# Kernel optimization log

Hardware: AMD Instinct MI355X
Metric: run time of the kernel (lower is better)

The kernel has to match this reference:

```python
import jax, jax.numpy as jnp
import numpy as np

N_NODES = 100000
N_EDGES = 1200000
NFEAT = 64
NHID = 64
NCLASS = 16
BN_EPS = 1e-5
L2_EPS = 1e-12


def setup_inputs() -> dict:
    key = jax.random.key(0)
    ks = jax.random.split(key, 8)
    edge_index = jax.random.randint(ks[0], (2, N_EDGES), 0, N_NODES, dtype=jnp.int64)
    x = jax.random.normal(ks[1], (N_NODES, NFEAT), dtype=jnp.float32)
    # SAGEConv params: lin_l (neighbor path, has bias), lin_r (root path, no bias)
    W_l = jax.random.normal(ks[2], (NHID, NFEAT), dtype=jnp.float32) * (1.0 / np.sqrt(NFEAT))
    b_l = jnp.zeros((NHID,), dtype=jnp.float32)
    W_r = jax.random.normal(ks[3], (NHID, NFEAT), dtype=jnp.float32) * (1.0 / np.sqrt(NFEAT))
    # BatchNorm1d affine params
    gamma = jnp.ones((NHID,), dtype=jnp.float32)
    beta = jnp.zeros((NHID,), dtype=jnp.float32)
    # final fc (xavier-ish scale, zero bias per weights_init)
    W_fc = jax.random.normal(ks[4], (NCLASS, NHID), dtype=jnp.float32) * (1.0 / np.sqrt(NHID))
    b_fc = jnp.zeros((NCLASS,), dtype=jnp.float32)
    return {"edge_index": edge_index, "x": x, "W_l": W_l, "b_l": b_l,
            "W_r": W_r, "gamma": gamma, "beta": beta, "W_fc": W_fc, "b_fc": b_fc}


def reference(edge_index, x, W_l, b_l, W_r, gamma, beta, W_fc, b_fc):
    N = x.shape[0]
    src, dst = edge_index[0], edge_index[1]
    # SAGEConv mean aggregation: gather x at source nodes, scatter-mean to dst
    msgs = x[src]                                                  # [E, F]
    sums = jax.ops.segment_sum(msgs, dst, num_segments=N)         # [N, F]
    cnt = jax.ops.segment_sum(jnp.ones((src.shape[0], 1), x.dtype), dst, num_segments=N)
    mean = sums / jnp.maximum(cnt, 1.0)
    # out = lin_l(mean_neighbors) + lin_r(x_root)
    h = mean @ W_l.T + b_l + x @ W_r.T                              # [N, H]
    # normalize=True -> L2 normalize rows (F.normalize semantics)
    h = h / jnp.maximum(jnp.linalg.norm(h, axis=-1, keepdims=True), L2_EPS)
    # transition: ReLU -> BatchNorm1d (training stats) -> Dropout (identity in eval)
    h = jax.nn.relu(h)
    mu = jnp.mean(h, axis=0)
    var = jnp.var(h, axis=0)
    h = (h - mu) / jnp.sqrt(var + BN_EPS) * gamma + beta
    return h @ W_fc.T + b_fc                                        # [N, C]
```

## Files before the change

### kernel.cpp

```cpp
#include <hip/hip_runtime.h>
#include <hip/hip_bf16.h>


typedef __attribute__((ext_vector_type(8))) short short8;
typedef __attribute__((ext_vector_type(4))) float f32x4;

__device__ __forceinline__ unsigned short f2bf(float f) {
    unsigned int u = __builtin_bit_cast(unsigned int, f);
    u += 0x7FFFu + ((u >> 16) & 1u);
    return (unsigned short)(u >> 16);
}
__device__ __forceinline__ float bf2f(unsigned short s) {
    return __builtin_bit_cast(float, ((unsigned int)s) << 16);
}

#define CHUNK 8192

__global__ __launch_bounds__(256) void k_bhist(const int* __restrict__ eidx,
                                               int* __restrict__ cnt,
                                               int E, int NB) {
    __shared__ int lh[256];
    const int tid = threadIdx.x;
    lh[tid] = 0;
    __syncthreads();
    const int base = blockIdx.x * CHUNK;
    for (int i = tid; i < CHUNK; i += 256) {
        int e = base + i;
        if (e < E) atomicAdd(&lh[eidx[E + e] >> 9], 1);
    }
    __syncthreads();
    if (tid < NB) cnt[(size_t)blockIdx.x * NB + tid] = lh[tid];
}

__global__ __launch_bounds__(256) void k_bscanA(int* __restrict__ cnt,
                                                int* __restrict__ btot,
                                                int NBLK, int NB) {
    __shared__ int swv[4];
    const int b = blockIdx.x;
    const int t = threadIdx.x;
    int v = (t < NBLK) ? cnt[(size_t)t * NB + b] : 0;
    const int lane = t & 63, wid = t >> 6;
    int s = v;
#pragma unroll
    for (int off = 1; off < 64; off <<= 1) {
        int tt = __shfl_up(s, off);
        if (lane >= off) s += tt;
    }
    if (lane == 63) swv[wid] = s;
    __syncthreads();
    if (t == 0) {
        int a = 0;
#pragma unroll
        for (int w = 0; w < 4; ++w) { int tt = swv[w]; swv[w] = a; a += tt; }
    }
    __syncthreads();
    int excl = s - v + swv[wid];
    if (t < NBLK) cnt[(size_t)t * NB + b] = excl;
    if (t == NBLK - 1) btot[b] = excl + v;
}

__global__ __launch_bounds__(256) void k_bscanB(const int* __restrict__ btot,
                                                int* __restrict__ bbase,
                                                int* __restrict__ rowptr,
                                                int NB, int N, int E) {
    __shared__ int swv[4];
    const int t = threadIdx.x;
    int v = (t < NB) ? btot[t] : 0;
    const int lane = t & 63, wid = t >> 6;
    int s = v;
#pragma unroll
    for (int off = 1; off < 64; off <<= 1) {
        int tt = __shfl_up(s, off);
        if (lane >= off) s += tt;
    }
    if (lane == 63) swv[wid] = s;
    __syncthreads();
    if (t == 0) {
        int a = 0;
#pragma unroll
        for (int w = 0; w < 4; ++w) { int tt = swv[w]; swv[w] = a; a += tt; }
    }
    __syncthreads();
    if (t < NB) bbase[t] = s - v + swv[wid];
    if (t == 0) { bbase[NB] = E; rowptr[N] = E; }
}

__global__ __launch_bounds__(256) void k_bscatter(const int* __restrict__ eidx,
                                                  const int* __restrict__ cnt,
                                                  const int* __restrict__ bbase,
                                                  unsigned int* __restrict__ ebuf,
                                                  int E, int NB) {
    __shared__ int cur[256];
    const int tid = threadIdx.x;
    if (tid < NB) cur[tid] = bbase[tid] + cnt[(size_t)blockIdx.x * NB + tid];
    __syncthreads();
    const int base = blockIdx.x * CHUNK;
    for (int i = tid; i < CHUNK; i += 256) {
        int e = base + i;
        if (e < E) {
            int d = eidx[E + e];
            int s = eidx[e];
            int p = atomicAdd(&cur[d >> 9], 1);
            ebuf[p] = (unsigned int)s | ((unsigned int)(d & 511) << 17);
        }
    }
}

__global__ __launch_bounds__(256) void k_bfinal(const unsigned int* __restrict__ ebuf,
                                                const int* __restrict__ bbase,
                                                int* __restrict__ rowptr,
                                                int* __restrict__ colv, int N) {
    __shared__ int h[512];
    __shared__ int swv[4];
    const int b = blockIdx.x;
    const int tid = threadIdx.x;
    h[2 * tid] = 0;
    h[2 * tid + 1] = 0;
    __syncthreads();
    const int segb = bbase[b], sege = bbase[b + 1];
    for (int i = segb + tid; i < sege; i += 256)
        atomicAdd(&h[ebuf[i] >> 17], 1);
    __syncthreads();
    int a0 = h[2 * tid], a1 = h[2 * tid + 1];
    int ts = a0 + a1;
    const int lane = tid & 63, wid = tid >> 6;
    int s = ts;
#pragma unroll
    for (int off = 1; off < 64; off <<= 1) {
        int tt = __shfl_up(s, off);
        if (lane >= off) s += tt;
    }
    if (lane == 63) swv[wid] = s;
    __syncthreads();
    if (tid == 0) {
        int a = 0;
#pragma unroll
        for (int w = 0; w < 4; ++w) { int tt = swv[w]; swv[w] = a; a += tt; }
    }
    __syncthreads();
    int excl = s - ts + swv[wid];
    h[2 * tid] = excl;
    h[2 * tid + 1] = excl + a0;
    int node = b * 512 + 2 * tid;
    if (node < N) rowptr[node] = segb + excl;
    if (node + 1 < N) rowptr[node + 1] = segb + excl + a0;
    __syncthreads();
    for (int i = segb + tid; i < sege; i += 256) {
        unsigned int u = ebuf[i];
        int p = atomicAdd(&h[u >> 17], 1);
        colv[segb + p] = (int)(u & 0x1FFFFu);
    }
}

__global__ __launch_bounds__(256) void k_xcast(const float4* __restrict__ x4,
                                               ushort4* __restrict__ xbf, int n4) {
    int t = blockIdx.x * 256 + threadIdx.x;
    if (t < n4) {
        float4 v = x4[t];
        xbf[t] = make_ushort4(f2bf(v.x), f2bf(v.y), f2bf(v.z), f2bf(v.w));
    }
}

__global__ __launch_bounds__(256) void k_gather_bf(
        const uint4* __restrict__ xbf8, const int* __restrict__ rowptr,
        const int* __restrict__ colv, uint4* __restrict__ mh8, int N) {
    int t = blockIdx.x * 256 + threadIdx.x;
    int n = t >> 3;
    int l = t & 7;
    if (n >= N) return;
    int b = rowptr[n], e = rowptr[n + 1];
    float a[8] = {0.f, 0.f, 0.f, 0.f, 0.f, 0.f, 0.f, 0.f};
    int p = b;
    for (; p + 4 <= e; p += 4) {
        int s0 = colv[p], s1 = colv[p + 1], s2 = colv[p + 2], s3 = colv[p + 3];
        uint4 v0 = xbf8[(size_t)s0 * 8 + l];
        uint4 v1 = xbf8[(size_t)s1 * 8 + l];
        uint4 v2 = xbf8[(size_t)s2 * 8 + l];
        uint4 v3 = xbf8[(size_t)s3 * 8 + l];
        unsigned int w0[4] = {v0.x, v0.y, v0.z, v0.w};
        unsigned int w1[4] = {v1.x, v1.y, v1.z, v1.w};
        unsigned int w2[4] = {v2.x, v2.y, v2.z, v2.w};
        unsigned int w3[4] = {v3.x, v3.y, v3.z, v3.w};
#pragma unroll
        for (int q = 0; q < 4; ++q) {
            a[2 * q] += bf2f((unsigned short)(w0[q] & 0xFFFF)) +
                        bf2f((unsigned short)(w1[q] & 0xFFFF)) +
                        bf2f((unsigned short)(w2[q] & 0xFFFF)) +
                        bf2f((unsigned short)(w3[q] & 0xFFFF));
            a[2 * q + 1] += bf2f((unsigned short)(w0[q] >> 16)) +
                            bf2f((unsigned short)(w1[q] >> 16)) +
                            bf2f((unsigned short)(w2[q] >> 16)) +
                            bf2f((unsigned short)(w3[q] >> 16));
        }
    }
    for (; p < e; ++p) {
        int s0 = colv[p];
        uint4 v0 = xbf8[(size_t)s0 * 8 + l];
        unsigned int w0[4] = {v0.x, v0.y, v0.z, v0.w};
#pragma unroll
        for (int q = 0; q < 4; ++q) {
            a[2 * q] += bf2f((unsigned short)(w0[q] & 0xFFFF));
            a[2 * q + 1] += bf2f((unsigned short)(w0[q] >> 16));
        }
    }
    float inv = 1.0f / fmaxf((float)(e - b), 1.0f);
    uint4 o;
    unsigned int* op = &o.x;
#pragma unroll
    for (int q = 0; q < 4; ++q) {
        unsigned int lo = f2bf(a[2 * q] * inv);
        unsigned int hi = f2bf(a[2 * q + 1] * inv);
        op[q] = lo | (hi << 16);
    }
    mh8[(size_t)n * 8 + l] = o;
}

__global__ __launch_bounds__(256) void k_gather_f32(
        const float4* __restrict__ x4, const int* __restrict__ rowptr,
        const int* __restrict__ colv, ushort4* __restrict__ mh, int N) {
    int t = blockIdx.x * 256 + threadIdx.x;
    int n = t >> 4;
    int l = t & 15;
    if (n >= N) return;
    int b = rowptr[n], e = rowptr[n + 1];
    float ax = 0.f, ay = 0.f, az = 0.f, aw = 0.f;
    int p = b;
    for (; p + 4 <= e; p += 4) {
        int s0 = colv[p], s1 = colv[p + 1], s2 = colv[p + 2], s3 = colv[p + 3];
        float4 v0 = x4[(size_t)s0 * 16 + l];
        float4 v1 = x4[(size_t)s1 * 16 + l];
        float4 v2 = x4[(size_t)s2 * 16 + l];
        float4 v3 = x4[(size_t)s3 * 16 + l];
        ax += (v0.x + v1.x) + (v2.x + v3.x);
        ay += (v0.y + v1.y) + (v2.y + v3.y);
        az += (v0.z + v1.z) + (v2.z + v3.z);
        aw += (v0.w + v1.w) + (v2.w + v3.w);
    }
    for (; p < e; ++p) {
        int s0 = colv[p];
        float4 v0 = x4[(size_t)s0 * 16 + l];
        ax += v0.x; ay += v0.y; az += v0.z; aw += v0.w;
    }
    float inv = 1.0f / fmaxf((float)(e - b), 1.0f);
    mh[(size_t)n * 16 + l] = make_ushort4(f2bf(ax * inv), f2bf(ay * inv),
                                          f2bf(az * inv), f2bf(aw * inv));
}

__global__ __launch_bounds__(256) void k_fused(
        const float* __restrict__ x,
        const float* __restrict__ Wl, const float* __restrict__ bl,
        const float* __restrict__ Wr,
        unsigned short* __restrict__ mh,
        float* __restrict__ pstats, int N) {
    __shared__ float sRed[4][128];

    const int tid = threadIdx.x;
    const int wid = tid >> 6;
    const int lane = tid & 63;
    const int l15 = lane & 15;
    const int quad = lane >> 4;
    const int tbase = blockIdx.x * 64 + wid * 16;

    short8 bfrag[4][4];
#pragma unroll
    for (int c = 0; c < 4; ++c) {
#pragma unroll
        for (int f = 0; f < 4; ++f) {
            const int n = f * 16 + l15;
            const float* wsrc = (c < 2)
                ? (Wl + (size_t)n * 64 + c * 32 + quad * 8)
                : (Wr + (size_t)n * 64 + (c - 2) * 32 + quad * 8);
            float4 w0 = *(const float4*)wsrc;
            float4 w1 = *(const float4*)(wsrc + 4);
            union { short8 v; unsigned short u[8]; } pk;
            pk.u[0] = f2bf(w0.x); pk.u[1] = f2bf(w0.y);
            pk.u[2] = f2bf(w0.z); pk.u[3] = f2bf(w0.w);
            pk.u[4] = f2bf(w1.x); pk.u[5] = f2bf(w1.y);
            pk.u[6] = f2bf(w1.z); pk.u[7] = f2bf(w1.w);
            bfrag[c][f] = pk.v;
        }
    }

    const int mrow = tbase + l15;
    const int mld = (mrow < N) ? mrow : (N - 1);
    f32x4 acc[4] = {{0.f, 0.f, 0.f, 0.f}, {0.f, 0.f, 0.f, 0.f},
                    {0.f, 0.f, 0.f, 0.f}, {0.f, 0.f, 0.f, 0.f}};
#pragma unroll
    for (int c = 0; c < 2; ++c) {
        short8 a = *(const short8*)(mh + (size_t)mld * 64 + c * 32 + quad * 8);
#pragma unroll
        for (int f = 0; f < 4; ++f)
            acc[f] = __builtin_amdgcn_mfma_f32_16x16x32_bf16(a, bfrag[c][f], acc[f], 0, 0, 0);
    }
#pragma unroll
    for (int c = 2; c < 4; ++c) {
        const float* xp = x + (size_t)mld * 64 + (c - 2) * 32 + quad * 8;
        float4 a0 = *(const float4*)xp;
        float4 a1 = *(const float4*)(xp + 4);
        union { short8 v; unsigned short u[8]; } pk;
        pk.u[0] = f2bf(a0.x); pk.u[1] = f2bf(a0.y);
        pk.u[2] = f2bf(a0.z); pk.u[3] = f2bf(a0.w);
        pk.u[4] = f2bf(a1.x); pk.u[5] = f2bf(a1.y);
        pk.u[6] = f2bf(a1.z); pk.u[7] = f2bf(a1.w);
#pragma unroll
        for (int f = 0; f < 4; ++f)
            acc[f] = __builtin_amdgcn_mfma_f32_16x16x32_bf16(pk.v, bfrag[c][f], acc[f], 0, 0, 0);
    }

    float blv[4];
#pragma unroll
    for (int f = 0; f < 4; ++f) blv[f] = bl[f * 16 + l15];

    float psum[4] = {0.f, 0.f, 0.f, 0.f};
    float psq[4] = {0.f, 0.f, 0.f, 0.f};
#pragma unroll
    for (int reg = 0; reg < 4; ++reg) {
        const int node = tbase + quad * 4 + reg;
        float hv[4];
        float ss = 0.f;
#pragma unroll
        for (int f = 0; f < 4; ++f) {
            hv[f] = acc[f][reg] + blv[f];
            ss += hv[f] * hv[f];
        }
        ss += __shfl_xor(ss, 1);
        ss += __shfl_xor(ss, 2);
        ss += __shfl_xor(ss, 4);
        ss += __shfl_xor(ss, 8);
        float sc = 1.0f / fmaxf(sqrtf(ss), 1e-12f);
        if (node < N) {
#pragma unroll
            for (int f = 0; f < 4; ++f) {
                float r = fmaxf(hv[f] * sc, 0.f);
                unsigned short rb = f2bf(r);
                float e = bf2f(rb);
                mh[(size_t)node * 64 + f * 16 + l15] = rb;
                psum[f] += e;
                psq[f] += e * e;
            }
        }
    }

#pragma unroll
    for (int f = 0; f < 4; ++f) {
        psum[f] += __shfl_xor(psum[f], 16);
        psum[f] += __shfl_xor(psum[f], 32);
        psq[f] += __shfl_xor(psq[f], 16);
        psq[f] += __shfl_xor(psq[f], 32);
    }
    if (lane < 16) {
#pragma unroll
        for (int f = 0; f < 4; ++f) {
            sRed[wid][f * 16 + l15] = psum[f];
            sRed[wid][64 + f * 16 + l15] = psq[f];
        }
    }
    __syncthreads();
    if (tid < 128) {
        float v = sRed[0][tid] + sRed[1][tid] + sRed[2][tid] + sRed[3][tid];
        pstats[(size_t)blockIdx.x * 128 + tid] = v;
    }
}

__global__ __launch_bounds__(64) void k_stats(const float* __restrict__ pstats,
                                              float* __restrict__ stats, int nblk) {
    int col = blockIdx.x;
    int l = threadIdx.x;
    float s = 0.f;
    for (int r = l; r < nblk; r += 64) s += pstats[(size_t)r * 128 + col];
    s += __shfl_xor(s, 1);
    s += __shfl_xor(s, 2);
    s += __shfl_xor(s, 4);
    s += __shfl_xor(s, 8);
    s += __shfl_xor(s, 16);
    s += __shfl_xor(s, 32);
    if (l == 0) stats[col] = s;
}

__global__ __launch_bounds__(256) void k_out(
        const unsigned short* __restrict__ h, const float* __restrict__ stats,
        const float* __restrict__ gamma, const float* __restrict__ beta,
        const float* __restrict__ Wfc, const float* __restrict__ bfc,
        float* __restrict__ out, int N) {
    __shared__ float sWm[64 * 16];
    __shared__ float sShift[64];
    __shared__ float sBase[16];
    const int tid = threadIdx.x;
    const float invN = 1.0f / (float)N;
    if (tid < 64) {
        float mu = stats[tid] * invN;
        float var = stats[64 + tid] * invN - mu * mu;
        float sc = gamma[tid] / sqrtf(var + 1e-5f);
        sShift[tid] = beta[tid] - mu * sc;
#pragma unroll
        for (int c = 0; c < 16; ++c) sWm[tid * 16 + c] = Wfc[c * 64 + tid] * sc;
    }
    __syncthreads();
    if (tid < 16) {
        float b = bfc[tid];
#pragma unroll
        for (int j = 0; j < 64; ++j) b += sShift[j] * Wfc[tid * 64 + j];
        sBase[tid] = b;
    }
    __syncthreads();
    int g = blockIdx.x * 256 + tid;
    int n = g >> 4;
    int c = g & 15;
    if (n >= N) return;
    const ushort4* h4 = (const ushort4*)(h + (size_t)n * 64);
    float acc = sBase[c];
#pragma unroll
    for (int jq = 0; jq < 16; ++jq) {
        ushort4 v = h4[jq];
        acc += bf2f(v.x) * sWm[(jq * 4 + 0) * 16 + c];
        acc += bf2f(v.y) * sWm[(jq * 4 + 1) * 16 + c];
        acc += bf2f(v.z) * sWm[(jq * 4 + 2) * 16 + c];
        acc += bf2f(v.w) * sWm[(jq * 4 + 3) * 16 + c];
    }
    out[(size_t)n * 16 + c] = acc;
}

extern "C" void kernel_launch(void* const* d_in, const int* in_sizes, int n_in,
                              void* d_out, int out_size, void* d_ws, size_t ws_size,
                              hipStream_t stream) {
    const int* eidx = (const int*)d_in[0];
    const float* x = (const float*)d_in[1];
    const float* Wl = (const float*)d_in[2];
    const float* bl = (const float*)d_in[3];
    const float* Wr = (const float*)d_in[4];
    const float* gamma = (const float*)d_in[5];
    const float* beta = (const float*)d_in[6];
    const float* Wfc = (const float*)d_in[7];
    const float* bfc = (const float*)d_in[8];
    float* out = (float*)d_out;

    const int E = in_sizes[0] / 2;
    const int N = in_sizes[1] / 64;
    const int fblocks = (N + 63) / 64;
    const int NB = (N + 511) >> 9;
    const int NBLK = (E + CHUNK - 1) / CHUNK;

    int* colv = (int*)d_ws;
    int* rowptr = colv + E;
    int* cnt = rowptr + (N + 1);
    int* btot = cnt + (size_t)NBLK * NB;
    int* bbase = btot + 256;
    float* pstats = (float*)(bbase + 257);
    float* stats = pstats + (size_t)fblocks * 128;
    unsigned short* mh = (unsigned short*)(stats + 128);
    unsigned int* tail = (unsigned int*)(mh + (size_t)N * 64);

    size_t fixed_words = (size_t)(tail - (unsigned int*)d_ws);
    const bool xbf_on = (ws_size >= (fixed_words + (size_t)N * 32) * 4);
    unsigned short* xbf = (unsigned short*)tail;
    unsigned int* ebuf = tail;

    int eblocks = (E + 255) / 256;
    k_bhist<<<NBLK, 256, 0, stream>>>(eidx, cnt, E, NB);
    k_bscanA<<<NB, 256, 0, stream>>>(cnt, btot, NBLK, NB);
    k_bscanB<<<1, 256, 0, stream>>>(btot, bbase, rowptr, NB, N, E);
    k_bscatter<<<NBLK, 256, 0, stream>>>(eidx, cnt, bbase, ebuf, E, NB);
    k_bfinal<<<NB, 256, 0, stream>>>(ebuf, bbase, rowptr, colv, N);

    if (xbf_on) {
        int cblocks = (int)(((size_t)N * 16 + 255) / 256);
        k_xcast<<<cblocks, 256, 0, stream>>>((const float4*)x, (ushort4*)xbf, N * 16);
        int gblocks = (int)(((size_t)N * 8 + 255) / 256);
        k_gather_bf<<<gblocks, 256, 0, stream>>>((const uint4*)xbf, rowptr, colv,
                                                 (uint4*)mh, N);
    } else {
        int gblocks = (int)(((size_t)N * 16 + 255) / 256);
        k_gather_f32<<<gblocks, 256, 0, stream>>>((const float4*)x, rowptr, colv,
                                                  (ushort4*)mh, N);
    }

    k_fused<<<fblocks, 256, 0, stream>>>(x, Wl, bl, Wr, mh, pstats, N);

    k_stats<<<128, 64, 0, stream>>>(pstats, stats, fblocks);

    int oblocks = (int)(((size_t)N * 16 + 255) / 256);
    k_out<<<oblocks, 256, 0, stream>>>(mh, stats, gamma, beta, Wfc, bfc, out, N);
}
```

Baseline: 236.0 us.

## Fuse CSR finalize with neighbor gather in shared memory and merge prep kernels

```diff
diff --git a/kernel.cpp b/kernel.cpp
--- a/kernel.cpp
+++ b/kernel.cpp
@@ -13,34 +13,53 @@
 __device__ __forceinline__ float bf2f(unsigned short s) {
     return __builtin_bit_cast(float, ((unsigned int)s) << 16);
 }
+__device__ __forceinline__ float bflo(unsigned int w) {
+    return __builtin_bit_cast(float, w << 16);
+}
+__device__ __forceinline__ float bfhi(unsigned int w) {
+    return __builtin_bit_cast(float, w & 0xFFFF0000u);
+}
 
 #define CHUNK 8192
-
-__global__ __launch_bounds__(256) void k_bhist(const int* __restrict__ eidx,
-                                               int* __restrict__ cnt,
-                                               int E, int NB) {
+#define MAXSEG 8192
+
+__global__ __launch_bounds__(256) void k_prep(const int* __restrict__ eidx,
+                                              int* __restrict__ cnt,
+                                              const float4* __restrict__ x4,
+                                              ushort4* __restrict__ xbf,
+                                              int E, int NB, int NBLK,
+                                              int n4, int do_x) {
     __shared__ int lh[256];
     const int tid = threadIdx.x;
-    lh[tid] = 0;
-    __syncthreads();
-    const int base = blockIdx.x * CHUNK;
-    for (int i = tid; i < CHUNK; i += 256) {
-        int e = base + i;
-        if (e < E) atomicAdd(&lh[eidx[E + e] >> 9], 1);
-    }
-    __syncthreads();
-    if (tid < NB) cnt[(size_t)blockIdx.x * NB + tid] = lh[tid];
-}
-
-__global__ __launch_bounds__(256) void k_bscanA(int* __restrict__ cnt,
-                                                int* __restrict__ btot,
-                                                int NBLK, int NB) {
+    if ((int)blockIdx.x < NBLK) {
+        lh[tid] = 0;
+        __syncthreads();
+        const int base = blockIdx.x * CHUNK;
+        for (int i = tid; i < CHUNK; i += 256) {
+            int e = base + i;
+            if (e < E) atomicAdd(&lh[eidx[E + e] >> 9], 1);
+        }
+        __syncthreads();
+        if (tid < NB) cnt[(size_t)blockIdx.x * NB + tid] = lh[tid];
+    } else if (do_x) {
+        int t = ((int)blockIdx.x - NBLK) * 256 + tid;
+        if (t < n4) {
+            float4 v = x4[t];
+            xbf[t] = make_ushort4(f2bf(v.x), f2bf(v.y), f2bf(v.z), f2bf(v.w));
+        }
+    }
+}
+
+__global__ __launch_bounds__(256) void k_bscan(int* __restrict__ cnt,
+                                               int* __restrict__ bbase,
+                                               int NBLK, int NB, int E) {
     __shared__ int swv[4];
-    const int b = blockIdx.x;
     const int t = threadIdx.x;
-    int v = (t < NBLK) ? cnt[(size_t)t * NB + b] : 0;
+    int tot = 0;
+    if (t < NB)
+        for (int c = 0; c < NBLK; ++c) tot += cnt[(size_t)c * NB + t];
     const int lane = t & 63, wid = t >> 6;
-    int s = v;
+    int s = tot;
 #pragma unroll
     for (int off = 1; off < 64; off <<= 1) {
         int tt = __shfl_up(s, off);
@@ -54,45 +73,26 @@
         for (int w = 0; w < 4; ++w) { int tt = swv[w]; swv[w] = a; a += tt; }
     }
     __syncthreads();
-    int excl = s - v + swv[wid];
-    if (t < NBLK) cnt[(size_t)t * NB + b] = excl;
-    if (t == NBLK - 1) btot[b] = excl + v;
-}
-
-__global__ __launch_bounds__(256) void k_bscanB(const int* __restrict__ btot,
-                                                int* __restrict__ bbase,
-                                                int* __restrict__ rowptr,
-                                                int NB, int N, int E) {
-    __shared__ int swv[4];
-    const int t = threadIdx.x;
-    int v = (t < NB) ? btot[t] : 0;
-    const int lane = t & 63, wid = t >> 6;
-    int s = v;
-#pragma unroll
-    for (int off = 1; off < 64; off <<= 1) {
-        int tt = __shfl_up(s, off);
-        if (lane >= off) s += tt;
-    }
-    if (lane == 63) swv[wid] = s;
-    __syncthreads();
-    if (t == 0) {
-        int a = 0;
-#pragma unroll
-        for (int w = 0; w < 4; ++w) { int tt = swv[w]; swv[w] = a; a += tt; }
-    }
-    __syncthreads();
-    if (t < NB) bbase[t] = s - v + swv[wid];
-    if (t == 0) { bbase[NB] = E; rowptr[N] = E; }
+    int base = s - tot + swv[wid];
+    if (t < NB) {
+        bbase[t] = base;
+        int run = base;
+        for (int c = 0; c < NBLK; ++c) {
+            int v = cnt[(size_t)c * NB + t];
+            cnt[(size_t)c * NB + t] = run;
+            run += v;
+        }
+    }
+    if (t == 0) bbase[NB] = E;
 }
 
 __global__ __launch_bounds__(256) void k_bscatter(const int* __restrict__ eidx,
                                                   const int* __restrict__ cnt,
-                                                  const int* __restrict__ bbase,
                                                   unsigned int* __restrict__ ebuf,
                                                   int E, int NB) {
     __shared__ int cur[256];
     const int tid = threadIdx.x;
-    if (tid < NB) cur[tid] = bbase[tid] + cnt[(size_t)blockIdx.x * NB + tid];
+    if (tid < NB) cur[tid] = cnt[(size_t)blockIdx.x * NB + tid];
     __syncthreads();
     const int base = blockIdx.x * CHUNK;
     for (int i = tid; i < CHUNK; i += 256) {
@@ -106,148 +106,125 @@
     }
 }
 
-__global__ __launch_bounds__(256) void k_bfinal(const unsigned int* __restrict__ ebuf,
+__global__ __launch_bounds__(256) void k_bucket(const unsigned int* __restrict__ ebuf,
                                                 const int* __restrict__ bbase,
-                                                int* __restrict__ rowptr,
-                                                int* __restrict__ colv, int N) {
-    __shared__ int h[512];
+                                                const uint2* __restrict__ xbf2,
+                                                const float4* __restrict__ x4,
+                                                uint2* __restrict__ mh2,
+                                                int N, int use_bf) {
+    __shared__ int lh[512];
+    __shared__ int lcur[512];
+    __shared__ int srcl[MAXSEG];
     __shared__ int swv[4];
     const int b = blockIdx.x;
     const int tid = threadIdx.x;
-    h[2 * tid] = 0;
-    h[2 * tid + 1] = 0;
-    __syncthreads();
     const int segb = bbase[b], sege = bbase[b + 1];
+    const int seg = sege - segb;
+    lh[2 * tid] = 0;
+    lh[2 * tid + 1] = 0;
+    __syncthreads();
     for (int i = segb + tid; i < sege; i += 256)
-        atomicAdd(&h[ebuf[i] >> 17], 1);
-    __syncthreads();
-    int a0 = h[2 * tid], a1 = h[2 * tid + 1];
-    int ts = a0 + a1;
-    const int lane = tid & 63, wid = tid >> 6;
-    int s = ts;
-#pragma unroll
-    for (int off = 1; off < 64; off <<= 1) {
-        int tt = __shfl_up(s, off);
-        if (lane >= off) s += tt;
-    }
-    if (lane == 63) swv[wid] = s;
-    __syncthreads();
-    if (tid == 0) {
-        int a = 0;
-#pragma unroll
-        for (int w = 0; w < 4; ++w) { int tt = swv[w]; swv[w] = a; a += tt; }
-    }
-    __syncthreads();
-    int excl = s - ts + swv[wid];
-    h[2 * tid] = excl;
-    h[2 * tid + 1] = excl + a0;
-    int node = b * 512 + 2 * tid;
-    if (node < N) rowptr[node] = segb + excl;
-    if (node + 1 < N) rowptr[node + 1] = segb + excl + a0;
-    __syncthreads();
-    for (int i = segb + tid; i < sege; i += 256) {
-        unsigned int u = ebuf[i];
-        int p = atomicAdd(&h[u >> 17], 1);
-        colv[segb + p] = (int)(u & 0x1FFFFu);
-    }
-}
-
-__global__ __launch_bounds__(256) void k_xcast(const float4* __restrict__ x4,
-                                               ushort4* __restrict__ xbf, int n4) {
-    int t = blockIdx.x * 256 + threadIdx.x;
-    if (t < n4) {
-        float4 v = x4[t];
-        xbf[t] = make_ushort4(f2bf(v.x), f2bf(v.y), f2bf(v.z), f2bf(v.w));
-    }
-}
-
-__global__ __launch_bounds__(256) void k_gather_bf(
-        const uint4* __restrict__ xbf8, const int* __restrict__ rowptr,
-        const int* __restrict__ colv, uint4* __restrict__ mh8, int N) {
-    int t = blockIdx.x * 256 + threadIdx.x;
-    int n = t >> 3;
-    int l = t & 7;
-    if (n >= N) return;
-    int b = rowptr[n], e = rowptr[n + 1];
-    float a[8] = {0.f, 0.f, 0.f, 0.f, 0.f, 0.f, 0.f, 0.f};
-    int p = b;
-    for (; p + 4 <= e; p += 4) {
-        int s0 = colv[p], s1 = colv[p + 1], s2 = colv[p + 2], s3 = colv[p + 3];
-        uint4 v0 = xbf8[(size_t)s0 * 8 + l];
-        uint4 v1 = xbf8[(size_t)s1 * 8 + l];
-        uint4 v2 = xbf8[(size_t)s2 * 8 + l];
-        uint4 v3 = xbf8[(size_t)s3 * 8 + l];
-        unsigned int w0[4] = {v0.x, v0.y, v0.z, v0.w};
-        unsigned int w1[4] = {v1.x, v1.y, v1.z, v1.w};
-        unsigned int w2[4] = {v2.x, v2.y, v2.z, v2.w};
-        unsigned int w3[4] = {v3.x, v3.y, v3.z, v3.w};
-#pragma unroll
-        for (int q = 0; q < 4; ++q) {
-            a[2 * q] += bf2f((unsigned short)(w0[q] & 0xFFFF)) +
-                        bf2f((unsigned short)(w1[q] & 0xFFFF)) +
-                        bf2f((unsigned short)(w2[q] & 0xFFFF)) +
-                        bf2f((unsigned short)(w3[q] & 0xFFFF));
-            a[2 * q + 1] += bf2f((unsigned short)(w0[q] >> 16)) +
-                            bf2f((unsigned short)(w1[q] >> 16)) +
-                            bf2f((unsigned short)(w2[q] >> 16)) +
-                            bf2f((unsigned short)(w3[q] >> 16));
-        }
-    }
-    for (; p < e; ++p) {
-        int s0 = colv[p];
-        uint4 v0 = xbf8[(size_t)s0 * 8 + l];
-        unsigned int w0[4] = {v0.x, v0.y, v0.z, v0.w};
-#pragma unroll
-        for (int q = 0; q < 4; ++q) {
-            a[2 * q] += bf2f((unsigned short)(w0[q] & 0xFFFF));
-            a[2 * q + 1] += bf2f((unsigned short)(w0[q] >> 16));
-        }
-    }
-    float inv = 1.0f / fmaxf((float)(e - b), 1.0f);
-    uint4 o;
-    unsigned int* op = &o.x;
-#pragma unroll
-    for (int q = 0; q < 4; ++q) {
-        unsigned int lo = f2bf(a[2 * q] * inv);
-        unsigned int hi = f2bf(a[2 * q + 1] * inv);
-        op[q] = lo | (hi << 16);
-    }
-    mh8[(size_t)n * 8 + l] = o;
-}
-
-__global__ __launch_bounds__(256) void k_gather_f32(
-        const float4* __restrict__ x4, const int* __restrict__ rowptr,
-        const int* __restrict__ colv, ushort4* __restrict__ mh, int N) {
-    int t = blockIdx.x * 256 + threadIdx.x;
-    int n = t >> 4;
-    int l = t & 15;
-    if (n >= N) return;
-    int b = rowptr[n], e = rowptr[n + 1];
-    float ax = 0.f, ay = 0.f, az = 0.f, aw = 0.f;
-    int p = b;
-    for (; p + 4 <= e; p += 4) {
-        int s0 = colv[p], s1 = colv[p + 1], s2 = colv[p + 2], s3 = colv[p + 3];
-        float4 v0 = x4[(size_t)s0 * 16 + l];
-        float4 v1 = x4[(size_t)s1 * 16 + l];
-        float4 v2 = x4[(size_t)s2 * 16 + l];
-        float4 v3 = x4[(size_t)s3 * 16 + l];
-        ax += (v0.x + v1.x) + (v2.x + v3.x);
-        ay += (v0.y + v1.y) + (v2.y + v3.y);
-        az += (v0.z + v1.z) + (v2.z + v3.z);
-        aw += (v0.w + v1.w) + (v2.w + v3.w);
-    }
-    for (; p < e; ++p) {
-        int s0 = colv[p];
-        float4 v0 = x4[(size_t)s0 * 16 + l];
-        ax += v0.x; ay += v0.y; az += v0.z; aw += v0.w;
-    }
-    float inv = 1.0f / fmaxf((float)(e - b), 1.0f);
-    mh[(size_t)n * 16 + l] = make_ushort4(f2bf(ax * inv), f2bf(ay * inv),
-                                          f2bf(az * inv), f2bf(aw * inv));
+        atomicAdd(&lh[ebuf[i] >> 17], 1);
+    __syncthreads();
+
+    const bool fast = (seg <= MAXSEG);
+    if (fast) {
+        int a0 = lh[2 * tid], a1 = lh[2 * tid + 1];
+        int ts = a0 + a1;
+        const int lane = tid & 63, wid = tid >> 6;
+        int s = ts;
+#pragma unroll
+        for (int off = 1; off < 64; off <<= 1) {
+            int tt = __shfl_up(s, off);
+            if (lane >= off) s += tt;
+        }
+        if (lane == 63) swv[wid] = s;
+        __syncthreads();
+        if (tid == 0) {
+            int a = 0;
+#pragma unroll
+            for (int w = 0; w < 4; ++w) { int tt = swv[w]; swv[w] = a; a += tt; }
+        }
+        __syncthreads();
+        int excl = s - ts + swv[wid];
+        lcur[2 * tid] = excl;
+        lcur[2 * tid + 1] = excl + a0;
+        __syncthreads();
+        for (int i = segb + tid; i < sege; i += 256) {
+            unsigned int u = ebuf[i];
+            int p = atomicAdd(&lcur[u >> 17], 1);
+            srcl[p] = (int)(u & 0x1FFFFu);
+        }
+        __syncthreads();
+    }
+
+    const int g = tid >> 4;
+    const int l = tid & 15;
+    for (int k = 0; k < 32; ++k) {
+        const int nl = g * 32 + k;
+        const int node = b * 512 + nl;
+        if (node >= N) break;
+        const int dg = lh[nl];
+        float a0 = 0.f, a1 = 0.f, a2 = 0.f, a3 = 0.f;
+        if (fast) {
+            const int end = lcur[nl];
+            int p = end - dg;
+            for (; p + 2 <= end; p += 2) {
+                int s0 = srcl[p], s1 = srcl[p + 1];
+                if (use_bf) {
+                    uint2 v0 = xbf2[(size_t)s0 * 16 + l];
+                    uint2 v1 = xbf2[(size_t)s1 * 16 + l];
+                    a0 += bflo(v0.x) + bflo(v1.x);
+                    a1 += bfhi(v0.x) + bfhi(v1.x);
+                    a2 += bflo(v0.y) + bflo(v1.y);
+                    a3 += bfhi(v0.y) + bfhi(v1.y);
+                } else {
+                    float4 v0 = x4[(size_t)s0 * 16 + l];
+                    float4 v1 = x4[(size_t)s1 * 16 + l];
+                    a0 += v0.x + v1.x; a1 += v0.y + v1.y;
+                    a2 += v0.z + v1.z; a3 += v0.w + v1.w;
+                }
+            }
+            if (p < end) {
+                int s0 = srcl[p];
+                if (use_bf) {
+                    uint2 v0 = xbf2[(size_t)s0 * 16 + l];
+                    a0 += bflo(v0.x); a1 += bfhi(v0.x);
+                    a2 += bflo(v0.y); a3 += bfhi(v0.y);
+                } else {
+                    float4 v0 = x4[(size_t)s0 * 16 + l];
+                    a0 += v0.x; a1 += v0.y; a2 += v0.z; a3 += v0.w;
+                }
+            }
+        } else {
+            for (int i = segb; i < sege; ++i) {
+                unsigned int u = ebuf[i];
+                if ((int)(u >> 17) == nl) {
+                    int s0 = (int)(u & 0x1FFFFu);
+                    if (use_bf) {
+                        uint2 v0 = xbf2[(size_t)s0 * 16 + l];
+                        a0 += bflo(v0.x); a1 += bfhi(v0.x);
+                        a2 += bflo(v0.y); a3 += bfhi(v0.y);
+                    } else {
+                        float4 v0 = x4[(size_t)s0 * 16 + l];
+                        a0 += v0.x; a1 += v0.y; a2 += v0.z; a3 += v0.w;
+                    }
+                }
+            }
+        }
+        float inv = 1.0f / fmaxf((float)dg, 1.0f);
+        unsigned int lo0 = f2bf(a0 * inv), hi0 = f2bf(a1 * inv);
+        unsigned int lo1 = f2bf(a2 * inv), hi1 = f2bf(a3 * inv);
+        uint2 o;
+        o.x = lo0 | (hi0 << 16);
+        o.y = lo1 | (hi1 << 16);
+        mh2[(size_t)node * 16 + l] = o;
+    }
 }
 
 __global__ __launch_bounds__(256) void k_fused(
         const float* __restrict__ x,
+        const unsigned short* __restrict__ xbf, int use_bf,
         const float* __restrict__ Wl, const float* __restrict__ bl,
         const float* __restrict__ Wr,
         unsigned short* __restrict__ mh,
@@ -259,7 +236,6 @@
     const int lane = tid & 63;
     const int l15 = lane & 15;
     const int quad = lane >> 4;
-    const int tbase = blockIdx.x * 64 + wid * 16;
 
     short8 bfrag[4][4];
 #pragma unroll
@@ -281,62 +257,76 @@
         }
     }
 
-    const int mrow = tbase + l15;
-    const int mld = (mrow < N) ? mrow : (N - 1);
-    f32x4 acc[4] = {{0.f, 0.f, 0.f, 0.f}, {0.f, 0.f, 0.f, 0.f},
-                    {0.f, 0.f, 0.f, 0.f}, {0.f, 0.f, 0.f, 0.f}};
-#pragma unroll
-    for (int c = 0; c < 2; ++c) {
-        short8 a = *(const short8*)(mh + (size_t)mld * 64 + c * 32 + quad * 8);
-#pragma unroll
-        for (int f = 0; f < 4; ++f)
-            acc[f] = __builtin_amdgcn_mfma_f32_16x16x32_bf16(a, bfrag[c][f], acc[f], 0, 0, 0);
-    }
-#pragma unroll
-    for (int c = 2; c < 4; ++c) {
-        const float* xp = x + (size_t)mld * 64 + (c - 2) * 32 + quad * 8;
-        float4 a0 = *(const float4*)xp;
-        float4 a1 = *(const float4*)(xp + 4);
-        union { short8 v; unsigned short u[8]; } pk;
-        pk.u[0] = f2bf(a0.x); pk.u[1] = f2bf(a0.y);
-        pk.u[2] = f2bf(a0.z); pk.u[3] = f2bf(a0.w);
-        pk.u[4] = f2bf(a1.x); pk.u[5] = f2bf(a1.y);
-        pk.u[6] = f2bf(a1.z); pk.u[7] = f2bf(a1.w);
-#pragma unroll
-        for (int f = 0; f < 4; ++f)
-            acc[f] = __builtin_amdgcn_mfma_f32_16x16x32_bf16(pk.v, bfrag[c][f], acc[f], 0, 0, 0);
-    }
-
     float blv[4];
 #pragma unroll
     for (int f = 0; f < 4; ++f) blv[f] = bl[f * 16 + l15];
 
     float psum[4] = {0.f, 0.f, 0.f, 0.f};
     float psq[4] = {0.f, 0.f, 0.f, 0.f};
-#pragma unroll
-    for (int reg = 0; reg < 4; ++reg) {
-        const int node = tbase + quad * 4 + reg;
-        float hv[4];
-        float ss = 0.f;
-#pragma unroll
-        for (int f = 0; f < 4; ++f) {
-            hv[f] = acc[f][reg] + blv[f];
-            ss += hv[f] * hv[f];
-        }
-        ss += __shfl_xor(ss, 1);
-        ss += __shfl_xor(ss, 2);
-        ss += __shfl_xor(ss, 4);
-        ss += __shfl_xor(ss, 8);
-        float sc = 1.0f / fmaxf(sqrtf(ss), 1e-12f);
-        if (node < N) {
+
+    for (int t4 = 0; t4 < 4; ++t4) {
+        const int tbase = blockIdx.x * 256 + wid * 64 + t4 * 16;
+        const int mrow = tbase + l15;
+        const int mld = (mrow < N) ? mrow : (N - 1);
+        f32x4 acc[4] = {{0.f, 0.f, 0.f, 0.f}, {0.f, 0.f, 0.f, 0.f},
+                        {0.f, 0.f, 0.f, 0.f}, {0.f, 0.f, 0.f, 0.f}};
+#pragma unroll
+        for (int c = 0; c < 2; ++c) {
+            short8 a = *(const short8*)(mh + (size_t)mld * 64 + c * 32 + quad * 8);
+#pragma unroll
+            for (int f = 0; f < 4; ++f)
+                acc[f] = __builtin_amdgcn_mfma_f32_16x16x32_bf16(a, bfrag[c][f], acc[f], 0, 0, 0);
+        }
+        if (use_bf) {
+#pragma unroll
+            for (int c = 0; c < 2; ++c) {
+                short8 a = *(const short8*)(xbf + (size_t)mld * 64 + c * 32 + quad * 8);
+#pragma unroll
+                for (int f = 0; f < 4; ++f)
+                    acc[f] = __builtin_amdgcn_mfma_f32_16x16x32_bf16(a, bfrag[c + 2][f], acc[f], 0, 0, 0);
+            }
+        } else {
+#pragma unroll
+            for (int c = 0; c < 2; ++c) {
+                const float* xp = x + (size_t)mld * 64 + c * 32 + quad * 8;
+                float4 a0 = *(const float4*)xp;
+                float4 a1 = *(const float4*)(xp + 4);
+                union { short8 v; unsigned short u[8]; } pk;
+                pk.u[0] = f2bf(a0.x); pk.u[1] = f2bf(a0.y);
+                pk.u[2] = f2bf(a0.z); pk.u[3] = f2bf(a0.w);
+                pk.u[4] = f2bf(a1.x); pk.u[5] = f2bf(a1.y);
+                pk.u[6] = f2bf(a1.z); pk.u[7] = f2bf(a1.w);
+#pragma unroll
+                for (int f = 0; f < 4; ++f)
+                    acc[f] = __builtin_amdgcn_mfma_f32_16x16x32_bf16(pk.v, bfrag[c + 2][f], acc[f], 0, 0, 0);
+            }
+        }
+
+#pragma unroll
+        for (int reg = 0; reg < 4; ++reg) {
+            const int node = tbase + quad * 4 + reg;
+            float hv[4];
+            float ss = 0.f;
 #pragma unroll
             for (int f = 0; f < 4; ++f) {
-                float r = fmaxf(hv[f] * sc, 0.f);
-                unsigned short rb = f2bf(r);
-                float e = bf2f(rb);
-                mh[(size_t)node * 64 + f * 16 + l15] = rb;
-                psum[f] += e;
-                psq[f] += e * e;
+                hv[f] = acc[f][reg] + blv[f];
+                ss += hv[f] * hv[f];
+            }
+            ss += __shfl_xor(ss, 1);
+            ss += __shfl_xor(ss, 2);
+            ss += __shfl_xor(ss, 4);
+            ss += __shfl_xor(ss, 8);
+            float sc = 1.0f / fmaxf(sqrtf(ss), 1e-12f);
+            if (node < N) {
+#pragma unroll
+                for (int f = 0; f < 4; ++f) {
+                    float r = fmaxf(hv[f] * sc, 0.f);
+                    unsigned short rb = f2bf(r);
+                    float e = bf2f(rb);
+                    mh[(size_t)node * 64 + f * 16 + l15] = rb;
+                    psum[f] += e;
+                    psq[f] += e * e;
+                }
             }
         }
     }
@@ -436,47 +426,31 @@
 
     const int E = in_sizes[0] / 2;
     const int N = in_sizes[1] / 64;
-    const int fblocks = (N + 63) / 64;
     const int NB = (N + 511) >> 9;
     const int NBLK = (E + CHUNK - 1) / CHUNK;
-
-    int* colv = (int*)d_ws;
-    int* rowptr = colv + E;
-    int* cnt = rowptr + (N + 1);
-    int* btot = cnt + (size_t)NBLK * NB;
-    int* bbase = btot + 256;
-    float* pstats = (float*)(bbase + 257);
-    float* stats = pstats + (size_t)fblocks * 128;
-    unsigned short* mh = (unsigned short*)(stats + 128);
-    unsigned int* tail = (unsigned int*)(mh + (size_t)N * 64);
-
-    size_t fixed_words = (size_t)(tail - (unsigned int*)d_ws);
-    const bool xbf_on = (ws_size >= (fixed_words + (size_t)N * 32) * 4);
-    unsigned short* xbf = (unsigned short*)tail;
-    unsigned int* ebuf = tail;
-
-    int eblocks = (E + 255) / 256;
-    k_bhist<<<NBLK, 256, 0, stream>>>(eidx, cnt, E, NB);
-    k_bscanA<<<NB, 256, 0, stream>>>(cnt, btot, NBLK, NB);
-    k_bscanB<<<1, 256, 0, stream>>>(btot, bbase, rowptr, NB, N, E);
-    k_bscatter<<<NBLK, 256, 0, stream>>>(eidx, cnt, bbase, ebuf, E, NB);
-    k_bfinal<<<NB, 256, 0, stream>>>(ebuf, bbase, rowptr, colv, N);
-
-    if (xbf_on) {
-        int cblocks = (int)(((size_t)N * 16 + 255) / 256);
-        k_xcast<<<cblocks, 256, 0, stream>>>((const float4*)x, (ushort4*)xbf, N * 16);
-        int gblocks = (int)(((size_t)N * 8 + 255) / 256);
-        k_gather_bf<<<gblocks, 256, 0, stream>>>((const uint4*)xbf, rowptr, colv,
-                                                 (uint4*)mh, N);
-    } else {
-        int gblocks = (int)(((size_t)N * 16 + 255) / 256);
-        k_gather_f32<<<gblocks, 256, 0, stream>>>((const float4*)x, rowptr, colv,
-                                                  (ushort4*)mh, N);
-    }
-
-    k_fused<<<fblocks, 256, 0, stream>>>(x, Wl, bl, Wr, mh, pstats, N);
-
-    k_stats<<<128, 64, 0, stream>>>(pstats, stats, fblocks);
+    const int fb2 = (N + 255) / 256;
+    const int n4 = N * 16;
+
+    int* cnt = (int*)d_ws;
+    int* bbase = cnt + (size_t)NBLK * NB;
+    float* pstats = (float*)(bbase + NB + 1);
+    float* stats = pstats + (size_t)fb2 * 128;
+    unsigned int* ebuf = (unsigned int*)(stats + 128);
+    unsigned short* mh = (unsigned short*)(ebuf + E);
+    unsigned short* xbf = mh + (size_t)N * 64;
+
+    size_t need_bf = (size_t)((char*)(xbf + (size_t)N * 64) - (char*)d_ws);
+    const int use_bf = (ws_size >= need_bf) ? 1 : 0;
+
+    int cbl = use_bf ? (n4 + 255) / 256 : 0;
+    k_prep<<<NBLK + cbl, 256, 0, stream>>>(eidx, cnt, (const float4*)x,
+                                           (ushort4*)xbf, E, NB, NBLK, n4, use_bf);
+    k_bscan<<<1, 256, 0, stream>>>(cnt, bbase, NBLK, NB, E);
+    k_bscatter<<<NBLK, 256, 0, stream>>>(eidx, cnt, ebuf, E, NB);
+    k_bucket<<<NB, 256, 0, stream>>>(ebuf, bbase, (const uint2*)xbf,
+                                     (const float4*)x, (uint2*)mh, N, use_bf);
+    k_fused<<<fb2, 256, 0, stream>>>(x, xbf, use_bf, Wl, bl, Wr, mh, pstats, N);
+    k_stats<<<128, 64, 0, stream>>>(pstats, stats, fb2);
 
     int oblocks = (int)(((size_t)N * 16 + 255) / 256);
     k_out<<<oblocks, 256, 0, stream>>>(mh, stats, gamma, beta, Wfc, bfc, out, N);
```

Result: slower. 341.9 us (+44.9%).
